# Kernel tuning notes

Hardware: AMD Instinct MI355X
Metric: run time of the kernel (lower is better)

Reference implementation:

```python
import jax, jax.numpy as jnp
import numpy as np

N_EXPERTS = 64
TOP_K = 8
NORM_TOPK = True
SCALING = 1.0


def setup_inputs() -> dict:
    key = jax.random.key(0)
    logits = jax.random.normal(key, (524288, N_EXPERTS), dtype=jnp.float32)
    return {"logits": logits}


def reference(logits):
    # scoring_func == 'softmax': softmax over expert dim in float32
    routing_weights = jax.nn.softmax(logits.astype(jnp.float32), axis=1)
    # top-k experts per token: values and indices, sorted descending (matches torch.topk)
    topk_weights, topk_ids = jax.lax.top_k(routing_weights, TOP_K)  # [T, K]
    if NORM_TOPK:
        topk_weights = topk_weights / jnp.sum(topk_weights, axis=-1, keepdims=True)
    if SCALING != 1.0:
        topk_weights = topk_weights * SCALING
    # torch.histc(topk_ids, bins=E, min=0, max=E) == bincount over flat ids (float output)
    tokens_per_expert = jnp.zeros((N_EXPERTS,), dtype=jnp.float32).at[topk_ids.ravel()].add(1.0)
    return (logits, routing_weights, topk_weights, topk_ids, tokens_per_expert)
```

## Files before the change

### kernel.cpp

```cpp
#include <hip/hip_runtime.h>
#include <math.h>

#define NEXP 64
#define TOPK 8
#define TILE 128
#define PITCH 65
#define MAXGRID 1024

typedef float v4 __attribute__((ext_vector_type(4)));

__global__ __launch_bounds__(TILE) void router_kernel(
    const float* __restrict__ logits,
    float* __restrict__ out_logits,
    float* __restrict__ out_rw,
    float* __restrict__ out_tw,
    float* __restrict__ out_ti,
    float* __restrict__ out_hist,
    int nTiles)
{
    __shared__ float tile[TILE * PITCH];
    __shared__ float SrowInv[TILE];
    __shared__ float shist[NEXP];

    const int tid = threadIdx.x;
    if (tid < NEXP) shist[tid] = 0.0f;

    const int stride = gridDim.x;
    int tb = blockIdx.x;

    v4 pre[16];
    {
        const v4* g = (const v4*)logits + (long)tb * TILE * (NEXP / 4);
        #pragma unroll
        for (int k = 0; k < 16; ++k)
            pre[k] = __builtin_nontemporal_load(&g[tid + TILE * k]);
    }

    for (; tb < nTiles; tb += stride) {
        const long tokBase = (long)tb * TILE;

        v4* gpass = (v4*)out_logits + tokBase * (NEXP / 4);
        #pragma unroll
        for (int k = 0; k < 16; ++k) {
            int i = tid + TILE * k;
            v4 v = pre[k];
            __builtin_nontemporal_store(v, &gpass[i]);
            int r  = i >> 4;
            int c4 = (i & 15) << 2;
            float* b = &tile[r * PITCH + c4];
            b[0] = v.x; b[1] = v.y; b[2] = v.z; b[3] = v.w;
        }
        __syncthreads();

        int nb = tb + stride;
        if (nb < nTiles) {
            const v4* g = (const v4*)logits + (long)nb * TILE * (NEXP / 4);
            #pragma unroll
            for (int k = 0; k < 16; ++k)
                pre[k] = __builtin_nontemporal_load(&g[tid + TILE * k]);
        }

        const float* __restrict__ row = &tile[tid * PITCH];
        float vals[TOPK], ids[TOPK];
        #pragma unroll
        for (int j = 0; j < TOPK; ++j) { vals[j] = -INFINITY; ids[j] = 0.0f; }
        float ssum = 0.0f;

        #pragma unroll 8
        for (int e = 0; e < NEXP; ++e) {
            float x  = row[e];
            ssum += __expf(x);
            float fe = (float)e;
            bool c[TOPK];
            #pragma unroll
            for (int j = 0; j < TOPK; ++j) c[j] = x > vals[j];
            #pragma unroll
            for (int j = TOPK - 1; j >= 1; --j) {
                vals[j] = c[j] ? (c[j - 1] ? vals[j - 1] : x)  : vals[j];
                ids[j]  = c[j] ? (c[j - 1] ? ids[j - 1]  : fe) : ids[j];
            }
            vals[0] = c[0] ? x  : vals[0];
            ids[0]  = c[0] ? fe : ids[0];
        }
        SrowInv[tid] = 1.0f / ssum;

        float ew[TOPK];
        float tsum = 0.0f;
        #pragma unroll
        for (int j = 0; j < TOPK; ++j) { ew[j] = __expf(vals[j]); tsum += ew[j]; }
        const float tinv = 1.0f / tsum;

        const long tok = tokBase + tid;
        v4* twp = (v4*)out_tw + tok * 2;
        v4* tip = (v4*)out_ti + tok * 2;
        v4 w0 = { ew[0]*tinv, ew[1]*tinv, ew[2]*tinv, ew[3]*tinv };
        v4 w1 = { ew[4]*tinv, ew[5]*tinv, ew[6]*tinv, ew[7]*tinv };
        v4 i0 = { ids[0], ids[1], ids[2], ids[3] };
        v4 i1 = { ids[4], ids[5], ids[6], ids[7] };
        __builtin_nontemporal_store(w0, &twp[0]);
        __builtin_nontemporal_store(w1, &twp[1]);
        __builtin_nontemporal_store(i0, &tip[0]);
        __builtin_nontemporal_store(i1, &tip[1]);

        #pragma unroll
        for (int j = 0; j < TOPK; ++j)
            atomicAdd(&shist[(int)ids[j]], 1.0f);

        __syncthreads();

        v4* grw = (v4*)out_rw + tokBase * (NEXP / 4);
        #pragma unroll
        for (int k = 0; k < 16; ++k) {
            int i  = tid + TILE * k;
            int rr = i >> 4;
            int c4 = (i & 15) << 2;
            float si = SrowInv[rr];
            const float* b = &tile[rr * PITCH + c4];
            v4 w;
            w.x = __expf(b[0]) * si;
            w.y = __expf(b[1]) * si;
            w.z = __expf(b[2]) * si;
            w.w = __expf(b[3]) * si;
            __builtin_nontemporal_store(w, &grw[i]);
        }
        __syncthreads();
    }

    if (tid < NEXP) atomicAdd(&out_hist[tid], shist[tid]);
}

extern "C" void kernel_launch(void* const* d_in, const int* in_sizes, int n_in,
                              void* d_out, int out_size, void* d_ws, size_t ws_size,
                              hipStream_t stream) {
    const float* logits = (const float*)d_in[0];
    const long T = (long)in_sizes[0] / NEXP;

    float* out      = (float*)d_out;
    float* o_logits = out;
    float* o_rw     = out + T * NEXP;
    float* o_tw     = out + 2 * T * NEXP;
    float* o_ti     = o_tw + T * TOPK;
    float* o_hist   = o_ti + T * TOPK;

    (void)hipMemsetAsync(o_hist, 0, NEXP * sizeof(float), stream);

    const int nTiles = (int)(T / TILE);
    const int grid   = nTiles < MAXGRID ? nTiles : MAXGRID;
    router_kernel<<<grid, TILE, 0, stream>>>(logits, o_logits, o_rw, o_tw, o_ti,
                                             o_hist, nTiles);
}
```

Measured before the change: 104.1 us.

## Use single-wavefront tiles without barriers and reuse softmax exponentials via LDS

```diff
diff --git a/kernel.cpp b/kernel.cpp
--- a/kernel.cpp
+++ b/kernel.cpp
@@ -3,9 +3,9 @@
 
 #define NEXP 64
 #define TOPK 8
-#define TILE 128
-#define PITCH 65
-#define MAXGRID 1024
+#define TILE 64
+#define VPITCH 17
+#define MAXGRID 2048
 
 typedef float v4 __attribute__((ext_vector_type(4)));
 
@@ -18,22 +18,21 @@
     float* __restrict__ out_hist,
     int nTiles)
 {
-    __shared__ float tile[TILE * PITCH];
-    __shared__ float SrowInv[TILE];
+    __shared__ v4 tile[TILE * VPITCH];
     __shared__ float shist[NEXP];
 
-    const int tid = threadIdx.x;
-    if (tid < NEXP) shist[tid] = 0.0f;
+    const int l = threadIdx.x;
+    shist[l] = 0.0f;
 
     const int stride = gridDim.x;
     int tb = blockIdx.x;
 
     v4 pre[16];
     {
-        const v4* g = (const v4*)logits + (long)tb * TILE * (NEXP / 4);
+        const v4* g = (const v4*)logits + (long)tb * (TILE * NEXP / 4);
         #pragma unroll
         for (int k = 0; k < 16; ++k)
-            pre[k] = __builtin_nontemporal_load(&g[tid + TILE * k]);
+            pre[k] = __builtin_nontemporal_load(&g[l + TILE * k]);
     }
 
     for (; tb < nTiles; tb += stride) {
@@ -42,47 +41,53 @@
         v4* gpass = (v4*)out_logits + tokBase * (NEXP / 4);
         #pragma unroll
         for (int k = 0; k < 16; ++k) {
-            int i = tid + TILE * k;
+            int i = l + TILE * k;
             v4 v = pre[k];
             __builtin_nontemporal_store(v, &gpass[i]);
             int r  = i >> 4;
-            int c4 = (i & 15) << 2;
-            float* b = &tile[r * PITCH + c4];
-            b[0] = v.x; b[1] = v.y; b[2] = v.z; b[3] = v.w;
+            int cq = i & 15;
+            tile[r * VPITCH + cq] = v;
         }
-        __syncthreads();
 
         int nb = tb + stride;
         if (nb < nTiles) {
-            const v4* g = (const v4*)logits + (long)nb * TILE * (NEXP / 4);
+            const v4* g = (const v4*)logits + (long)nb * (TILE * NEXP / 4);
             #pragma unroll
             for (int k = 0; k < 16; ++k)
-                pre[k] = __builtin_nontemporal_load(&g[tid + TILE * k]);
+                pre[k] = __builtin_nontemporal_load(&g[l + TILE * k]);
         }
 
-        const float* __restrict__ row = &tile[tid * PITCH];
+        v4* row = &tile[l * VPITCH];
         float vals[TOPK], ids[TOPK];
         #pragma unroll
         for (int j = 0; j < TOPK; ++j) { vals[j] = -INFINITY; ids[j] = 0.0f; }
         float ssum = 0.0f;
 
-        #pragma unroll 8
-        for (int e = 0; e < NEXP; ++e) {
-            float x  = row[e];
-            ssum += __expf(x);
-            float fe = (float)e;
-            bool c[TOPK];
+        #pragma unroll
+        for (int q = 0; q < 16; ++q) {
+            v4 x4 = row[q];
+            v4 e4;
             #pragma unroll
-            for (int j = 0; j < TOPK; ++j) c[j] = x > vals[j];
-            #pragma unroll
-            for (int j = TOPK - 1; j >= 1; --j) {
-                vals[j] = c[j] ? (c[j - 1] ? vals[j - 1] : x)  : vals[j];
-                ids[j]  = c[j] ? (c[j - 1] ? ids[j - 1]  : fe) : ids[j];
+            for (int u = 0; u < 4; ++u) {
+                float x  = x4[u];
+                float ev = __expf(x);
+                ssum += ev;
+                e4[u] = ev;
+                float fe = (float)(q * 4 + u);
+                bool c[TOPK];
+                #pragma unroll
+                for (int j = 0; j < TOPK; ++j) c[j] = x > vals[j];
+                #pragma unroll
+                for (int j = TOPK - 1; j >= 1; --j) {
+                    ids[j]  = c[j] ? (c[j - 1] ? ids[j - 1] : fe) : ids[j];
+                    vals[j] = __builtin_amdgcn_fmed3f(x, vals[j - 1], vals[j]);
+                }
+                ids[0]  = c[0] ? fe : ids[0];
+                vals[0] = fmaxf(vals[0], x);
             }
-            vals[0] = c[0] ? x  : vals[0];
-            ids[0]  = c[0] ? fe : ids[0];
+            row[q] = e4;
         }
-        SrowInv[tid] = 1.0f / ssum;
+        const float sinv = 1.0f / ssum;
 
         float ew[TOPK];
         float tsum = 0.0f;
@@ -90,11 +95,11 @@
         for (int j = 0; j < TOPK; ++j) { ew[j] = __expf(vals[j]); tsum += ew[j]; }
         const float tinv = 1.0f / tsum;
 
-        const long tok = tokBase + tid;
+        const long tok = tokBase + l;
         v4* twp = (v4*)out_tw + tok * 2;
         v4* tip = (v4*)out_ti + tok * 2;
-        v4 w0 = { ew[0]*tinv, ew[1]*tinv, ew[2]*tinv, ew[3]*tinv };
-        v4 w1 = { ew[4]*tinv, ew[5]*tinv, ew[6]*tinv, ew[7]*tinv };
+        v4 w0 = { ew[0] * tinv, ew[1] * tinv, ew[2] * tinv, ew[3] * tinv };
+        v4 w1 = { ew[4] * tinv, ew[5] * tinv, ew[6] * tinv, ew[7] * tinv };
         v4 i0 = { ids[0], ids[1], ids[2], ids[3] };
         v4 i1 = { ids[4], ids[5], ids[6], ids[7] };
         __builtin_nontemporal_store(w0, &twp[0]);
@@ -106,27 +111,20 @@
         for (int j = 0; j < TOPK; ++j)
             atomicAdd(&shist[(int)ids[j]], 1.0f);
 
-        __syncthreads();
-
         v4* grw = (v4*)out_rw + tokBase * (NEXP / 4);
         #pragma unroll
         for (int k = 0; k < 16; ++k) {
-            int i  = tid + TILE * k;
+            int i  = l + TILE * k;
             int rr = i >> 4;
-            int c4 = (i & 15) << 2;
-            float si = SrowInv[rr];
-            const float* b = &tile[rr * PITCH + c4];
-            v4 w;
-            w.x = __expf(b[0]) * si;
-            w.y = __expf(b[1]) * si;
-            w.z = __expf(b[2]) * si;
-            w.w = __expf(b[3]) * si;
+            int cq = i & 15;
+            float si = __shfl(sinv, rr);
+            v4 w = tile[rr * VPITCH + cq];
+            w.x *= si; w.y *= si; w.z *= si; w.w *= si;
             __builtin_nontemporal_store(w, &grw[i]);
         }
-        __syncthreads();
     }
 
-    if (tid < NEXP) atomicAdd(&out_hist[tid], shist[tid]);
+    atomicAdd(&out_hist[l], shist[l]);
 }
 
 extern "C" void kernel_launch(void* const* d_in, const int* in_sizes, int n_in,
```

New measurement: 117.3 us. 12.7% more time.

## Make tiles wave-local, drop block barriers, process two tiles per block

Applied to the files above, without the earlier changes.

```diff
diff --git a/kernel.cpp b/kernel.cpp
--- a/kernel.cpp
+++ b/kernel.cpp
@@ -5,9 +5,102 @@
 #define TOPK 8
 #define TILE 128
 #define PITCH 65
-#define MAXGRID 1024
 
 typedef float v4 __attribute__((ext_vector_type(4)));
+
+__device__ __forceinline__ void stage_tile(const v4* __restrict__ buf,
+                                           v4* __restrict__ gpass,
+                                           float* __restrict__ tile,
+                                           int w, int l)
+{
+    #pragma unroll
+    for (int k = 0; k < 16; ++k) {
+        int i = (w << 10) + l + (k << 6);
+        v4 v = buf[k];
+        __builtin_nontemporal_store(v, &gpass[i]);
+        int r  = i >> 4;
+        int c4 = (i & 15) << 2;
+        float* b = &tile[r * PITCH + c4];
+        b[0] = v.x; b[1] = v.y; b[2] = v.z; b[3] = v.w;
+    }
+}
+
+__device__ __forceinline__ void load_tile(v4* __restrict__ buf,
+                                          const v4* __restrict__ g, int l)
+{
+    #pragma unroll
+    for (int k = 0; k < 16; ++k)
+        buf[k] = __builtin_nontemporal_load(&g[l + (k << 6)]);
+}
+
+__device__ __forceinline__ void compute_tile(const float* __restrict__ tile,
+                                             const v4* __restrict__ buf,
+                                             float* __restrict__ out_rw,
+                                             float* __restrict__ out_tw,
+                                             float* __restrict__ out_ti,
+                                             float* shist,
+                                             long tokBase, int w, int l, int tid)
+{
+    const float* __restrict__ row = &tile[tid * PITCH];
+    float vals[TOPK], ids[TOPK];
+    #pragma unroll
+    for (int j = 0; j < TOPK; ++j) { vals[j] = -INFINITY; ids[j] = 0.0f; }
+    float ssum = 0.0f;
+
+    #pragma unroll 8
+    for (int e = 0; e < NEXP; ++e) {
+        float x = row[e];
+        ssum += __expf(x);
+        float fe = (float)e;
+        bool c[TOPK];
+        #pragma unroll
+        for (int j = 0; j < TOPK; ++j) c[j] = x > vals[j];
+        #pragma unroll
+        for (int j = TOPK - 1; j >= 1; --j) {
+            ids[j]  = c[j] ? (c[j - 1] ? ids[j - 1] : fe) : ids[j];
+            vals[j] = __builtin_amdgcn_fmed3f(x, vals[j - 1], vals[j]);
+        }
+        ids[0]  = c[0] ? fe : ids[0];
+        vals[0] = fmaxf(vals[0], x);
+    }
+    const float sinv = 1.0f / ssum;
+
+    float ew[TOPK];
+    float tsum = 0.0f;
+    #pragma unroll
+    for (int j = 0; j < TOPK; ++j) { ew[j] = __expf(vals[j]); tsum += ew[j]; }
+    const float tinv = 1.0f / tsum;
+
+    const long tok = tokBase + tid;
+    v4* twp = (v4*)out_tw + tok * 2;
+    v4* tip = (v4*)out_ti + tok * 2;
+    v4 w0 = { ew[0] * tinv, ew[1] * tinv, ew[2] * tinv, ew[3] * tinv };
+    v4 w1 = { ew[4] * tinv, ew[5] * tinv, ew[6] * tinv, ew[7] * tinv };
+    v4 i0 = { ids[0], ids[1], ids[2], ids[3] };
+    v4 i1 = { ids[4], ids[5], ids[6], ids[7] };
+    __builtin_nontemporal_store(w0, &twp[0]);
+    __builtin_nontemporal_store(w1, &twp[1]);
+    __builtin_nontemporal_store(i0, &tip[0]);
+    __builtin_nontemporal_store(i1, &tip[1]);
+
+    #pragma unroll
+    for (int j = 0; j < TOPK; ++j)
+        atomicAdd(&shist[(int)ids[j]], 1.0f);
+
+    v4* grw = (v4*)out_rw + tokBase * (NEXP / 4);
+    #pragma unroll
+    for (int k = 0; k < 16; ++k) {
+        int i = (w << 10) + l + (k << 6);
+        float si = __shfl(sinv, (l >> 4) + 4 * k);
+        v4 x = buf[k];
+        v4 o;
+        o.x = __expf(x.x) * si;
+        o.y = __expf(x.y) * si;
+        o.z = __expf(x.z) * si;
+        o.w = __expf(x.w) * si;
+        __builtin_nontemporal_store(o, &grw[i]);
+    }
+}
 
 __global__ __launch_bounds__(TILE) void router_kernel(
     const float* __restrict__ logits,
@@ -19,113 +112,47 @@
     int nTiles)
 {
     __shared__ float tile[TILE * PITCH];
-    __shared__ float SrowInv[TILE];
     __shared__ float shist[NEXP];
 
     const int tid = threadIdx.x;
+    const int w   = tid >> 6;
+    const int l   = tid & 63;
     if (tid < NEXP) shist[tid] = 0.0f;
+    __syncthreads();
 
-    const int stride = gridDim.x;
-    int tb = blockIdx.x;
+    const int grid = gridDim.x;
+    const int tA = blockIdx.x;
+    const int tB = tA + grid;
 
-    v4 pre[16];
+    const long baseA = (long)tA * TILE;
+    v4 bufA[16], bufB[16];
+
+    load_tile(bufA, (const v4*)logits + baseA * (NEXP / 4), (w << 10) / 64 ? l : l);
     {
-        const v4* g = (const v4*)logits + (long)tb * TILE * (NEXP / 4);
+        const v4* gA = (const v4*)logits + baseA * (NEXP / 4) + (w << 10);
         #pragma unroll
         for (int k = 0; k < 16; ++k)
-            pre[k] = __builtin_nontemporal_load(&g[tid + TILE * k]);
+            bufA[k] = __builtin_nontemporal_load(&gA[l + (k << 6)]);
+    }
+    stage_tile(bufA, (v4*)out_logits + baseA * (NEXP / 4), tile, w, l);
+
+    const bool hasB = tB < nTiles;
+    const long baseB = (long)tB * TILE;
+    if (hasB) {
+        const v4* gB = (const v4*)logits + baseB * (NEXP / 4) + (w << 10);
+        #pragma unroll
+        for (int k = 0; k < 16; ++k)
+            bufB[k] = __builtin_nontemporal_load(&gB[l + (k << 6)]);
     }
 
-    for (; tb < nTiles; tb += stride) {
-        const long tokBase = (long)tb * TILE;
+    compute_tile(tile, bufA, out_rw, out_tw, out_ti, shist, baseA, w, l, tid);
 
-        v4* gpass = (v4*)out_logits + tokBase * (NEXP / 4);
-        #pragma unroll
-        for (int k = 0; k < 16; ++k) {
-            int i = tid + TILE * k;
-            v4 v = pre[k];
-            __builtin_nontemporal_store(v, &gpass[i]);
-            int r  = i >> 4;
-            int c4 = (i & 15) << 2;
-            float* b = &tile[r * PITCH + c4];
-            b[0] = v.x; b[1] = v.y; b[2] = v.z; b[3] = v.w;
-        }
-        __syncthreads();
-
-        int nb = tb + stride;
-        if (nb < nTiles) {
-            const v4* g = (const v4*)logits + (long)nb * TILE * (NEXP / 4);
-            #pragma unroll
-            for (int k = 0; k < 16; ++k)
-                pre[k] = __builtin_nontemporal_load(&g[tid + TILE * k]);
-        }
-
-        const float* __restrict__ row = &tile[tid * PITCH];
-        float vals[TOPK], ids[TOPK];
-        #pragma unroll
-        for (int j = 0; j < TOPK; ++j) { vals[j] = -INFINITY; ids[j] = 0.0f; }
-        float ssum = 0.0f;
-
-        #pragma unroll 8
-        for (int e = 0; e < NEXP; ++e) {
-            float x  = row[e];
-            ssum += __expf(x);
-            float fe = (float)e;
-            bool c[TOPK];
-            #pragma unroll
-            for (int j = 0; j < TOPK; ++j) c[j] = x > vals[j];
-            #pragma unroll
-            for (int j = TOPK - 1; j >= 1; --j) {
-                vals[j] = c[j] ? (c[j - 1] ? vals[j - 1] : x)  : vals[j];
-                ids[j]  = c[j] ? (c[j - 1] ? ids[j - 1]  : fe) : ids[j];
-            }
-            vals[0] = c[0] ? x  : vals[0];
-            ids[0]  = c[0] ? fe : ids[0];
-        }
-        SrowInv[tid] = 1.0f / ssum;
-
-        float ew[TOPK];
-        float tsum = 0.0f;
-        #pragma unroll
-        for (int j = 0; j < TOPK; ++j) { ew[j] = __expf(vals[j]); tsum += ew[j]; }
-        const float tinv = 1.0f / tsum;
-
-        const long tok = tokBase + tid;
-        v4* twp = (v4*)out_tw + tok * 2;
-        v4* tip = (v4*)out_ti + tok * 2;
-        v4 w0 = { ew[0]*tinv, ew[1]*tinv, ew[2]*tinv, ew[3]*tinv };
-        v4 w1 = { ew[4]*tinv, ew[5]*tinv, ew[6]*tinv, ew[7]*tinv };
-        v4 i0 = { ids[0], ids[1], ids[2], ids[3] };
-        v4 i1 = { ids[4], ids[5], ids[6], ids[7] };
-        __builtin_nontemporal_store(w0, &twp[0]);
-        __builtin_nontemporal_store(w1, &twp[1]);
-        __builtin_nontemporal_store(i0, &tip[0]);
-        __builtin_nontemporal_store(i1, &tip[1]);
-
-        #pragma unroll
-        for (int j = 0; j < TOPK; ++j)
-            atomicAdd(&shist[(int)ids[j]], 1.0f);
-
-        __syncthreads();
-
-        v4* grw = (v4*)out_rw + tokBase * (NEXP / 4);
-        #pragma unroll
-        for (int k = 0; k < 16; ++k) {
-            int i  = tid + TILE * k;
-            int rr = i >> 4;
-            int c4 = (i & 15) << 2;
-            float si = SrowInv[rr];
-            const float* b = &tile[rr * PITCH + c4];
-            v4 w;
-            w.x = __expf(b[0]) * si;
-            w.y = __expf(b[1]) * si;
-            w.z = __expf(b[2]) * si;
-            w.w = __expf(b[3]) * si;
-            __builtin_nontemporal_store(w, &grw[i]);
-        }
-        __syncthreads();
+    if (hasB) {
+        stage_tile(bufB, (v4*)out_logits + baseB * (NEXP / 4), tile, w, l);
+        compute_tile(tile, bufB, out_rw, out_tw, out_ti, shist, baseB, w, l, tid);
     }
 
+    __syncthreads();
     if (tid < NEXP) atomicAdd(&out_hist[tid], shist[tid]);
 }
 
@@ -145,7 +172,7 @@
     (void)hipMemsetAsync(o_hist, 0, NEXP * sizeof(float), stream);
 
     const int nTiles = (int)(T / TILE);
-    const int grid   = nTiles < MAXGRID ? nTiles : MAXGRID;
+    const int grid   = (nTiles + 1) / 2;
     router_kernel<<<grid, TILE, 0, stream>>>(logits, o_logits, o_rw, o_tw, o_ti,
                                              o_hist, nTiles);
 }
```

After: 109.0 us. 4.7% more time.
